# Kernel tuning notes

Measured on AMD Instinct MI355X. Metric: run time of the kernel, lower is better.

## Reference

```python
import jax, jax.numpy as jnp
import numpy as np

B, N, D, H = 128, 256, 256, 4  # batch, atoms, feature dim (= fingerprint = input = output), heads
NEG_BIG = -1e10


def setup_inputs() -> dict:
    key = jax.random.key(0)
    ks = jax.random.split(key, 8)
    atom_neighbor_SNN = jax.random.normal(ks[0], (B, N, D), dtype=jnp.float32)
    # 0/1 adjacency (float): mask trick exp(x*-1e10)*-1e10 expects binary entries
    x_full_atom_neighbors = jax.random.randint(ks[1], (B, N, N), 0, 2).astype(jnp.float32)
    # shared neighbor_fc: Linear(D, D)
    lim = 1.0 / np.sqrt(D)
    fc_w = jax.random.uniform(ks[2], (D, D), jnp.float32, -lim, lim)
    fc_b = jnp.zeros((D,), jnp.float32)
    # per-head kernels (xavier_uniform)
    xav = np.sqrt(6.0 / (D + D))
    kernels = jax.random.uniform(ks[3], (H, D, D), jnp.float32, -xav, xav)
    # attention kernels (2D, 1) split into self/neigh halves, xavier on (2D,1)
    xav_a = np.sqrt(6.0 / (2 * D + 1))
    att_self = jax.random.uniform(ks[4], (H, D), jnp.float32, -xav_a, xav_a)
    att_neigh = jax.random.uniform(ks[5], (H, D), jnp.float32, -xav_a, xav_a)
    epsilons = jnp.full((H,), 0.6, jnp.float32)
    biases = jnp.zeros((H, D), jnp.float32)
    att_biases = jnp.zeros((H,), jnp.float32)
    return {
        "atom_neighbor_SNN": atom_neighbor_SNN,
        "x_full_atom_neighbors": x_full_atom_neighbors,
        "fc_w": fc_w, "fc_b": fc_b,
        "kernels": kernels,
        "att_self": att_self, "att_neigh": att_neigh,
        "epsilons": epsilons, "biases": biases, "att_biases": att_biases,
    }


def reference(atom_neighbor_SNN, x_full_atom_neighbors, fc_w, fc_b, kernels,
              att_self, att_neigh, epsilons, biases, att_biases):
    x = x_full_atom_neighbors                      # [B,N,N]
    atom = atom_neighbor_SNN                       # [B,N,D]
    diag = jnp.diagonal(x, axis1=-2, axis2=-1)     # [B,N]
    # new_x[h] = x + eye*diag*(eps[h]-1); so new_x[h] @ atom = x@atom + (eps[h]-1)*diag[:,:,None]*atom
    base = jnp.einsum('bnm,bmd->bnd', x, atom)     # [B,N,D]
    diagterm = diag[..., None] * atom              # [B,N,D]
    nf = base[None] + (epsilons - 1.0)[:, None, None, None] * diagterm[None]  # [H,B,N,D]
    h = jax.nn.leaky_relu(jnp.einsum('hbnd,df->hbnf', nf, fc_w) + fc_b, 0.01)  # shared fc, leaky_relu
    feat = jnp.einsum('hbnf,hfo->hbno', h, kernels) + biases[:, None, None, :]  # [H,B,N,D]
    a_s = jnp.einsum('hbno,ho->hbn', feat, att_self) + att_biases[:, None, None]
    a_n = jnp.einsum('hbno,ho->hbn', feat, att_neigh)
    att = jax.nn.elu(a_s[..., :, None] + a_n[..., None, :])  # [H,B,N,N]
    mask = jnp.exp(x * NEG_BIG) * NEG_BIG                     # 0 on edges, -1e10 off edges
    att = jax.nn.softmax(att + mask[None], axis=-1)
    # dropout: identity (eval mode)
    node = jnp.einsum('hbij,hbjo->hbio', att, feat)           # [H,B,N,D]
    out = jnp.moveaxis(node, 0, 2).reshape(node.shape[1], node.shape[2], H * node.shape[3])  # concat heads -> [B,N,H*D]
    return out, att[-1]
```

## Files before the change

kernel.cpp:

```cpp
#include <hip/hip_runtime.h>

typedef __attribute__((ext_vector_type(8))) short bf16x8;
typedef __attribute__((ext_vector_type(4))) short short4v;
typedef __attribute__((ext_vector_type(4))) float f32x4;


__device__ __forceinline__ float b2f(short s){
  unsigned u = ((unsigned)(unsigned short)s) << 16;
  return __builtin_bit_cast(float, u);
}
__device__ __forceinline__ short f2b(float f){
  unsigned u = __builtin_bit_cast(unsigned, f);
  u = (u + 0x7FFFu + ((u >> 16) & 1u)) >> 16;
  return (short)(unsigned short)u;
}

#define SWZ(row, bytecol) ((((row) * 512) + (bytecol)) ^ (((row) & 7) << 4))

__global__ __launch_bounds__(256) void ktrans(const float* __restrict__ fcw, const float* __restrict__ kers,
                                              short* __restrict__ WT, short* __restrict__ KhT){
  __shared__ float tile[32][33];
  int z = blockIdx.z;
  const float* src = (z == 0) ? fcw : (kers + (z-1)*65536);
  short* dst = (z == 0) ? WT : (KhT + (z-1)*65536);
  int x0 = blockIdx.x*32, y0 = blockIdx.y*32;
  int tx = threadIdx.x & 31, ty = threadIdx.x >> 5;
  #pragma unroll
  for (int i = 0; i < 32; i += 8) tile[ty+i][tx] = src[(y0+ty+i)*256 + x0+tx];
  __syncthreads();
  #pragma unroll
  for (int i = 0; i < 32; i += 8) dst[(x0+ty+i)*256 + y0+tx] = f2b(tile[tx][ty+i]);
}

__global__ __launch_bounds__(512, 1) void kG12(const short* __restrict__ WT, const float* __restrict__ atom,
                                               const float* __restrict__ x,
                                               short* __restrict__ G2nf, short* __restrict__ G1,
                                               unsigned* __restrict__ xbits, float* __restrict__ diag){
  __shared__ __align__(16) char G2s[65536];
  int wg = blockIdx.x;
  int xcd = wg & 7, idx = wg >> 3;
  int b  = xcd + ((idx >> 1) << 3);
  int fh = idx & 1;
  int tid = threadIdx.x, lane = tid & 63, w = tid >> 6;
  int lr = lane & 15, lq = lane >> 4, koff = lq * 8;

  {
    int wm = (w >> 1) * 64, wf = (w & 1) * 64;
    const float* Ab = atom + b*65536;
    const short* Bw = WT + (fh*128 + wf)*256;
    f32x4 acc[4][4] = {};
    for (int k0 = 0; k0 < 256; k0 += 32){
      bf16x8 af[4], bfr[4];
      #pragma unroll
      for (int i = 0; i < 4; i++){
        const float* p = Ab + (wm + i*16 + lr)*256 + k0 + koff;
        f32x4 a0 = *(const f32x4*)p, a1 = *(const f32x4*)(p + 4);
        #pragma unroll
        for (int e = 0; e < 4; e++){ af[i][e] = f2b(a0[e]); af[i][4+e] = f2b(a1[e]); }
      }
      #pragma unroll
      for (int j = 0; j < 4; j++) bfr[j] = *(const bf16x8*)(Bw + (j*16 + lr)*256 + k0 + koff);
      #pragma unroll
      for (int i = 0; i < 4; i++)
        #pragma unroll
        for (int j = 0; j < 4; j++)
          acc[i][j] = __builtin_amdgcn_mfma_f32_16x16x32_bf16(af[i], bfr[j], acc[i][j], 0, 0, 0);
    }
    #pragma unroll
    for (int i = 0; i < 4; i++)
      #pragma unroll
      for (int j = 0; j < 4; j++){
        short4v v;
        #pragma unroll
        for (int r = 0; r < 4; r++) v[r] = f2b(acc[i][j][r]);
        int fl = wf + j*16 + lr;
        int m0 = wm + i*16 + lq*4;
        *(short4v*)(G2s + SWZ(fl, m0*2)) = v;
        #pragma unroll
        for (int r = 0; r < 4; r++)
          G2nf[b*65536 + (m0 + r)*256 + fh*128 + fl] = v[r];
      }
  }
  __syncthreads();

  {
    int wf2 = (w >> 2) * 64, wn2 = (w & 3) * 64;
    const float* Xb = x + b*65536;
    f32x4 acc[4][4] = {};
    for (int k0 = 0; k0 < 256; k0 += 32){
      bf16x8 af[4], bfr[4];
      #pragma unroll
      for (int i = 0; i < 4; i++) af[i]  = *(const bf16x8*)(G2s + SWZ(wf2 + i*16 + lr, (k0 + koff)*2));
      #pragma unroll
      for (int j = 0; j < 4; j++){
        int n = wn2 + j*16 + lr;
        const float* p = Xb + n*256 + k0 + koff;
        f32x4 x0 = *(const f32x4*)p, x1 = *(const f32x4*)(p + 4);
        unsigned b8 = 0u;
        #pragma unroll
        for (int e = 0; e < 4; e++){
          bfr[j][e] = f2b(x0[e]);     if (x0[e] > 0.5f) b8 |= (1u << e);
          bfr[j][4+e] = f2b(x1[e]);   if (x1[e] > 0.5f) b8 |= (1u << (4 + e));
        }
        if (w < 4){
          unsigned full = b8 << (lq * 8);
          full |= __shfl_xor(full, 16);
          full |= __shfl_xor(full, 32);
          if (lq == 0) xbits[(b*256 + n)*8 + (k0 >> 5)] = full;
          int nm = n & 31;
          if ((n & ~31) == k0 && (nm >> 3) == lq)
            diag[b*256 + n] = (nm & 4) ? x1[nm & 3] : x0[nm & 3];
        }
      }
      #pragma unroll
      for (int i = 0; i < 4; i++)
        #pragma unroll
        for (int j = 0; j < 4; j++)
          acc[i][j] = __builtin_amdgcn_mfma_f32_16x16x32_bf16(af[i], bfr[j], acc[i][j], 0, 0, 0);
    }
    #pragma unroll
    for (int i = 0; i < 4; i++)
      #pragma unroll
      for (int j = 0; j < 4; j++){
        short4v v;
        #pragma unroll
        for (int r = 0; r < 4; r++) v[r] = f2b(acc[i][j][r]);
        *(short4v*)(G1 + b*65536 + (wn2 + j*16 + lr)*256 + fh*128 + wf2 + i*16 + lq*4) = v;
      }
  }
}

__global__ __launch_bounds__(512, 1) void kHead(const short* __restrict__ KhT, const short* __restrict__ G1,
                                                const short* __restrict__ G2nf, const float* __restrict__ diag,
                                                const float* __restrict__ fcb, const float* __restrict__ epsv,
                                                const float* __restrict__ biases, const float* __restrict__ atts,
                                                const float* __restrict__ attn, const float* __restrict__ attbv,
                                                const unsigned* __restrict__ xbits,
                                                float* __restrict__ out, float* __restrict__ out2){
  __shared__ __align__(16) char featS[131072];
  __shared__ __align__(16) char scratch[24576];
  __shared__ float asvL[256], anvL[256], fcbL[256];

  short (*h1s)[40] = (short(*)[40])scratch;
  float (*red_s)[64] = (float(*)[64])(scratch);
  float (*red_n)[64] = (float(*)[64])(scratch + 2048);
  unsigned* xbitsL = (unsigned*)(scratch + 4096);

  int wg = blockIdx.x;
  int xcd = wg & 7, idx = wg >> 3;
  int b = xcd + ((idx >> 2) << 3);
  int h = idx & 3;
  int tid = threadIdx.x, lane = tid & 63, w = tid >> 6;
  float epsm1 = epsv[h] - 1.0f;
  const short* KA  = KhT + h*65536;
  const short* G1b = G1  + b*65536;
  const short* G2b = G2nf + b*65536;

  {
    int o = tid >> 1, half = (tid & 1) * 128;
    #pragma unroll
    for (int q = 0; q < 16; q++){
      int kk = half + q*8;
      bf16x8 v = *(const bf16x8*)(KA + o*256 + kk);
      *(bf16x8*)(featS + SWZ(o, kk*2)) = v;
    }
    if (tid < 256) fcbL[tid] = fcb[tid];
  }

  int nl = tid >> 1, rkk = (tid & 1) * 16;
  float cj = epsm1 * diag[b*256 + nl];

  int wro = (w >> 2) * 128;
  int wn  = (w & 3) * 64;
  int lr = lane & 15, lq = lane >> 4;
  int koff = lq * 8;

  bf16x8 p1a = *(const bf16x8*)(G1b + nl*256 + rkk);
  bf16x8 p1b = *(const bf16x8*)(G1b + nl*256 + rkk + 8);
  bf16x8 p2a = *(const bf16x8*)(G2b + nl*256 + rkk);
  bf16x8 p2b = *(const bf16x8*)(G2b + nl*256 + rkk + 8);

  __syncthreads();

  f32x4 acc[4][8] = {};
  for (int t = 0; t < 8; t++){
    int k0 = t*32;
    {
      bf16x8 o1, o2;
      #pragma unroll
      for (int e = 0; e < 8; e++){
        float v = b2f(p1a[e]) + cj*b2f(p2a[e]) + fcbL[k0 + rkk + e];
        v = v > 0.f ? v : 0.01f*v;
        o1[e] = f2b(v);
      }
      #pragma unroll
      for (int e = 0; e < 8; e++){
        float v = b2f(p1b[e]) + cj*b2f(p2b[e]) + fcbL[k0 + rkk + 8 + e];
        v = v > 0.f ? v : 0.01f*v;
        o2[e] = f2b(v);
      }
      *(bf16x8*)&h1s[nl][rkk] = o1;
      *(bf16x8*)&h1s[nl][rkk + 8] = o2;
    }
    __syncthreads();
    if (t < 7){
      int kn = k0 + 32;
      p1a = *(const bf16x8*)(G1b + nl*256 + kn + rkk);
      p1b = *(const bf16x8*)(G1b + nl*256 + kn + rkk + 8);
      p2a = *(const bf16x8*)(G2b + nl*256 + kn + rkk);
      p2b = *(const bf16x8*)(G2b + nl*256 + kn + rkk + 8);
    }
    bf16x8 af[4];
    #pragma unroll
    for (int j = 0; j < 4; j++) af[j] = *(const bf16x8*)&h1s[wn + j*16 + lr][koff];
    #pragma unroll
    for (int i = 0; i < 8; i++){
      bf16x8 bfv = *(const bf16x8*)(featS + SWZ(wro + i*16 + lr, (k0 + koff)*2));
      #pragma unroll
      for (int j = 0; j < 4; j++)
        acc[j][i] = __builtin_amdgcn_mfma_f32_16x16x32_bf16(af[j], bfv, acc[j][i], 0, 0, 0);
    }
    __syncthreads();
  }

  float ps[4][4] = {}, pn[4][4] = {};
  #pragma unroll
  for (int i = 0; i < 8; i++){
    int od = wro + i*16 + lr;
    float bi  = biases[h*256 + od];
    float wsv = atts[h*256 + od];
    float wnv = attn[h*256 + od];
    #pragma unroll
    for (int j = 0; j < 4; j++){
      short4v sv;
      #pragma unroll
      for (int r = 0; r < 4; r++){
        float fv = acc[j][i][r] + bi;
        sv[r] = f2b(fv);
        ps[j][r] += fv * wsv;
        pn[j][r] += fv * wnv;
      }
      *(short4v*)(featS + SWZ(od, (wn + j*16 + lq*4)*2) ) = sv;
    }
  }
  #pragma unroll
  for (int j = 0; j < 4; j++)
    #pragma unroll
    for (int r = 0; r < 4; r++){
      float s = ps[j][r], nv = pn[j][r];
      s += __shfl_xor(s, 1); s += __shfl_xor(s, 2); s += __shfl_xor(s, 4); s += __shfl_xor(s, 8);
      nv += __shfl_xor(nv, 1); nv += __shfl_xor(nv, 2); nv += __shfl_xor(nv, 4); nv += __shfl_xor(nv, 8);
      ps[j][r] = s; pn[j][r] = nv;
    }
  if (lr == 0){
    #pragma unroll
    for (int j = 0; j < 4; j++)
      #pragma unroll
      for (int r = 0; r < 4; r++){
        red_s[w][j*16 + lq*4 + r] = ps[j][r];
        red_n[w][j*16 + lq*4 + r] = pn[j][r];
      }
  }
  {
    const unsigned* xb = xbits + b*2048;
    #pragma unroll
    for (int q = 0; q < 4; q++) xbitsL[tid*4 + q] = xb[tid*4 + q];
  }
  __syncthreads();
  if (tid < 256){
    int q = tid >> 6, nn = tid & 63;
    asvL[tid] = red_s[q][nn] + red_s[q+4][nn] + attbv[h];
    anvL[tid] = red_n[q][nn] + red_n[q+4][nn];
  }
  __syncthreads();

  int wi = w * 32;
  bf16x8 bfp[2][8];
  #pragma unroll
  for (int sub = 0; sub < 2; sub++){
    int i = wi + sub*16 + lr;
    float as_i = asvL[i];
    float Lv[8][8];
    float mx = -3.0e38f;
    #pragma unroll
    for (int t = 0; t < 8; t++){
      unsigned bits = xbitsL[i*8 + t] >> (lq*8);
      #pragma unroll
      for (int e = 0; e < 8; e++){
        float s = as_i + anvL[t*32 + lq*8 + e];
        float el = s > 0.f ? s : (__expf(s) - 1.0f);
        float L = el + (((bits >> e) & 1u) ? 0.f : -1.0e10f);
        Lv[t][e] = L; mx = fmaxf(mx, L);
      }
    }
    mx = fmaxf(mx, __shfl_xor(mx, 16));
    mx = fmaxf(mx, __shfl_xor(mx, 32));
    float sum = 0.f;
    #pragma unroll
    for (int t = 0; t < 8; t++)
      #pragma unroll
      for (int e = 0; e < 8; e++){ float p = __expf(Lv[t][e] - mx); Lv[t][e] = p; sum += p; }
    sum += __shfl_xor(sum, 16);
    sum += __shfl_xor(sum, 32);
    float inv = 1.0f / sum;
    #pragma unroll
    for (int t = 0; t < 8; t++){
      bf16x8 pv;
      #pragma unroll
      for (int e = 0; e < 8; e++) pv[e] = f2b(Lv[t][e] * inv);
      bfp[sub][t] = pv;
    }
    if (h == 3){
      float* o2 = out2 + b*65536 + i*256 + lq*8;
      #pragma unroll
      for (int t = 0; t < 8; t++){
        f32x4 v0, v1;
        #pragma unroll
        for (int e = 0; e < 4; e++){ v0[e] = Lv[t][e]*inv; v1[e] = Lv[t][4+e]*inv; }
        *(f32x4*)(o2 + t*32) = v0;
        *(f32x4*)(o2 + t*32 + 4) = v1;
      }
    }
  }

  float* outb = out + (size_t)(b*256 + wi)*1024 + h*256;
  #pragma unroll 1
  for (int ot = 0; ot < 16; ot++){
    f32x4 a2[2] = {};
    #pragma unroll
    for (int t = 0; t < 8; t++){
      bf16x8 afv = *(const bf16x8*)(featS + SWZ(ot*16 + lr, (t*32 + lq*8)*2));
      a2[0] = __builtin_amdgcn_mfma_f32_16x16x32_bf16(afv, bfp[0][t], a2[0], 0, 0, 0);
      a2[1] = __builtin_amdgcn_mfma_f32_16x16x32_bf16(afv, bfp[1][t], a2[1], 0, 0, 0);
    }
    *(f32x4*)(outb + (size_t)(lr)*1024 + ot*16 + lq*4) = a2[0];
    *(f32x4*)(outb + (size_t)(16 + lr)*1024 + ot*16 + lq*4) = a2[1];
  }
}

extern "C" void kernel_launch(void* const* d_in, const int* in_sizes, int n_in,
                              void* d_out, int out_size, void* d_ws, size_t ws_size,
                              hipStream_t stream) {
  const float* atom   = (const float*)d_in[0];
  const float* x      = (const float*)d_in[1];
  const float* fc_w   = (const float*)d_in[2];
  const float* fc_b   = (const float*)d_in[3];
  const float* kers   = (const float*)d_in[4];
  const float* att_s  = (const float*)d_in[5];
  const float* att_n  = (const float*)d_in[6];
  const float* eps    = (const float*)d_in[7];
  const float* biases = (const float*)d_in[8];
  const float* att_b  = (const float*)d_in[9];

  char* w = (char*)d_ws;
  short* WT      = (short*)(w);
  short* KhT     = (short*)(w + 131072);
  float* diag    = (float*)(w + 655360);
  unsigned* xbits= (unsigned*)(w + 786432);
  short* G2nf    = (short*)(w + 1835008);
  short* G1      = (short*)(w + 18612224);

  float* out  = (float*)d_out;
  float* out2 = out + 33554432;

  ktrans<<<dim3(8, 8, 5), 256, 0, stream>>>(fc_w, kers, WT, KhT);
  kG12<<<dim3(256), 512, 0, stream>>>(WT, atom, x, G2nf, G1, xbits, diag);
  kHead<<<dim3(512), 512, 0, stream>>>(KhT, G1, G2nf, diag, fc_b, eps,
                                       biases, att_s, att_n, att_b, xbits, out, out2);
}
```

Baseline: 145.2 us.

## Split G12 over feature quarters and stage full activation tile in LDS for head GEMM

kG12 now splits the feature dimension into quarters instead of halves. That doubles the grid to 512 workgroups, halves the LDS staging buffer, and declares higher occupancy through launch bounds. kHead now computes the full leaky-relu activation tile (all 256 k) into LDS once up front and reads the per-head kernel weights straight from global memory. Previously the weights were staged in LDS and the activations were produced 32 columns at a time with two barriers per k-step. This removes the per-iteration synchronisation, at the cost of uncached global weight loads inside the MFMA loop and redundant recomputation of the atom-by-weight GEMM across the quarter splits.

```diff
diff --git a/kernel.cpp b/kernel.cpp
--- a/kernel.cpp
+++ b/kernel.cpp
@@ -32,25 +32,25 @@
   for (int i = 0; i < 32; i += 8) dst[(x0+ty+i)*256 + y0+tx] = f2b(tile[tx][ty+i]);
 }
 
-__global__ __launch_bounds__(512, 1) void kG12(const short* __restrict__ WT, const float* __restrict__ atom,
+__global__ __launch_bounds__(512, 4) void kG12(const short* __restrict__ WT, const float* __restrict__ atom,
                                                const float* __restrict__ x,
                                                short* __restrict__ G2nf, short* __restrict__ G1,
                                                unsigned* __restrict__ xbits, float* __restrict__ diag){
-  __shared__ __align__(16) char G2s[65536];
+  __shared__ __align__(16) char G2s[32768];
   int wg = blockIdx.x;
   int xcd = wg & 7, idx = wg >> 3;
-  int b  = xcd + ((idx >> 1) << 3);
-  int fh = idx & 1;
+  int b  = xcd + ((idx >> 2) << 3);
+  int fq = idx & 3;
   int tid = threadIdx.x, lane = tid & 63, w = tid >> 6;
   int lr = lane & 15, lq = lane >> 4, koff = lq * 8;
 
   {
-    int wm = (w >> 1) * 64, wf = (w & 1) * 64;
+    int wm = (w >> 1) * 64, wf = (w & 1) * 32;
     const float* Ab = atom + b*65536;
-    const short* Bw = WT + (fh*128 + wf)*256;
-    f32x4 acc[4][4] = {};
+    const short* Bw = WT + (fq*64 + wf)*256;
+    f32x4 acc[4][2] = {};
     for (int k0 = 0; k0 < 256; k0 += 32){
-      bf16x8 af[4], bfr[4];
+      bf16x8 af[4], bfr[2];
       #pragma unroll
       for (int i = 0; i < 4; i++){
         const float* p = Ab + (wm + i*16 + lr)*256 + k0 + koff;
@@ -59,17 +59,17 @@
         for (int e = 0; e < 4; e++){ af[i][e] = f2b(a0[e]); af[i][4+e] = f2b(a1[e]); }
       }
       #pragma unroll
-      for (int j = 0; j < 4; j++) bfr[j] = *(const bf16x8*)(Bw + (j*16 + lr)*256 + k0 + koff);
+      for (int j = 0; j < 2; j++) bfr[j] = *(const bf16x8*)(Bw + (j*16 + lr)*256 + k0 + koff);
       #pragma unroll
       for (int i = 0; i < 4; i++)
         #pragma unroll
-        for (int j = 0; j < 4; j++)
+        for (int j = 0; j < 2; j++)
           acc[i][j] = __builtin_amdgcn_mfma_f32_16x16x32_bf16(af[i], bfr[j], acc[i][j], 0, 0, 0);
     }
     #pragma unroll
     for (int i = 0; i < 4; i++)
       #pragma unroll
-      for (int j = 0; j < 4; j++){
+      for (int j = 0; j < 2; j++){
         short4v v;
         #pragma unroll
         for (int r = 0; r < 4; r++) v[r] = f2b(acc[i][j][r]);
@@ -78,19 +78,19 @@
         *(short4v*)(G2s + SWZ(fl, m0*2)) = v;
         #pragma unroll
         for (int r = 0; r < 4; r++)
-          G2nf[b*65536 + (m0 + r)*256 + fh*128 + fl] = v[r];
+          G2nf[b*65536 + (m0 + r)*256 + fq*64 + fl] = v[r];
       }
   }
   __syncthreads();
 
   {
-    int wf2 = (w >> 2) * 64, wn2 = (w & 3) * 64;
+    int wf2 = (w >> 2) * 32, wn2 = (w & 3) * 64;
     const float* Xb = x + b*65536;
-    f32x4 acc[4][4] = {};
+    f32x4 acc[2][4] = {};
     for (int k0 = 0; k0 < 256; k0 += 32){
-      bf16x8 af[4], bfr[4];
-      #pragma unroll
-      for (int i = 0; i < 4; i++) af[i]  = *(const bf16x8*)(G2s + SWZ(wf2 + i*16 + lr, (k0 + koff)*2));
+      bf16x8 af[2], bfr[4];
+      #pragma unroll
+      for (int i = 0; i < 2; i++) af[i] = *(const bf16x8*)(G2s + SWZ(wf2 + i*16 + lr, (k0 + koff)*2));
       #pragma unroll
       for (int j = 0; j < 4; j++){
         int n = wn2 + j*16 + lr;
@@ -113,19 +113,19 @@
         }
       }
       #pragma unroll
-      for (int i = 0; i < 4; i++)
+      for (int i = 0; i < 2; i++)
         #pragma unroll
         for (int j = 0; j < 4; j++)
           acc[i][j] = __builtin_amdgcn_mfma_f32_16x16x32_bf16(af[i], bfr[j], acc[i][j], 0, 0, 0);
     }
     #pragma unroll
-    for (int i = 0; i < 4; i++)
+    for (int i = 0; i < 2; i++)
       #pragma unroll
       for (int j = 0; j < 4; j++){
         short4v v;
         #pragma unroll
         for (int r = 0; r < 4; r++) v[r] = f2b(acc[i][j][r]);
-        *(short4v*)(G1 + b*65536 + (wn2 + j*16 + lr)*256 + fh*128 + wf2 + i*16 + lq*4) = v;
+        *(short4v*)(G1 + b*65536 + (wn2 + j*16 + lr)*256 + fq*64 + wf2 + i*16 + lq*4) = v;
       }
   }
 }
@@ -138,10 +138,9 @@
                                                 const unsigned* __restrict__ xbits,
                                                 float* __restrict__ out, float* __restrict__ out2){
   __shared__ __align__(16) char featS[131072];
-  __shared__ __align__(16) char scratch[24576];
-  __shared__ float asvL[256], anvL[256], fcbL[256];
-
-  short (*h1s)[40] = (short(*)[40])scratch;
+  __shared__ __align__(16) char scratch[12288];
+  __shared__ float asvL[256], anvL[256];
+
   float (*red_s)[64] = (float(*)[64])(scratch);
   float (*red_n)[64] = (float(*)[64])(scratch + 2048);
   unsigned* xbitsL = (unsigned*)(scratch + 4096);
@@ -157,71 +156,61 @@
   const short* G2b = G2nf + b*65536;
 
   {
-    int o = tid >> 1, half = (tid & 1) * 128;
-    #pragma unroll
-    for (int q = 0; q < 16; q++){
-      int kk = half + q*8;
-      bf16x8 v = *(const bf16x8*)(KA + o*256 + kk);
-      *(bf16x8*)(featS + SWZ(o, kk*2)) = v;
-    }
-    if (tid < 256) fcbL[tid] = fcb[tid];
-  }
-
-  int nl = tid >> 1, rkk = (tid & 1) * 16;
-  float cj = epsm1 * diag[b*256 + nl];
+    int nl = tid >> 1, rkk = (tid & 1) * 16;
+    float cj = epsm1 * diag[b*256 + nl];
+    #pragma unroll
+    for (int kb = 0; kb < 8; kb++){
+      int k0 = kb*32 + rkk;
+      bf16x8 g1a = *(const bf16x8*)(G1b + nl*256 + k0);
+      bf16x8 g1c = *(const bf16x8*)(G1b + nl*256 + k0 + 8);
+      bf16x8 g2a = *(const bf16x8*)(G2b + nl*256 + k0);
+      bf16x8 g2c = *(const bf16x8*)(G2b + nl*256 + k0 + 8);
+      f32x4 f0 = *(const f32x4*)(fcb + k0);
+      f32x4 f1 = *(const f32x4*)(fcb + k0 + 4);
+      f32x4 f2 = *(const f32x4*)(fcb + k0 + 8);
+      f32x4 f3 = *(const f32x4*)(fcb + k0 + 12);
+      bf16x8 o1, o2;
+      #pragma unroll
+      for (int e = 0; e < 8; e++){
+        float v = b2f(g1a[e]) + cj*b2f(g2a[e]) + ((e < 4) ? f0[e] : f1[e-4]);
+        v = v > 0.f ? v : 0.01f*v;
+        o1[e] = f2b(v);
+      }
+      #pragma unroll
+      for (int e = 0; e < 8; e++){
+        float v = b2f(g1c[e]) + cj*b2f(g2c[e]) + ((e < 4) ? f2[e] : f3[e-4]);
+        v = v > 0.f ? v : 0.01f*v;
+        o2[e] = f2b(v);
+      }
+      *(bf16x8*)(featS + SWZ(nl, k0*2)) = o1;
+      *(bf16x8*)(featS + SWZ(nl, k0*2 + 16)) = o2;
+    }
+    const unsigned* xb = xbits + b*2048;
+    #pragma unroll
+    for (int q = 0; q < 4; q++) xbitsL[tid*4 + q] = xb[tid*4 + q];
+  }
+  __syncthreads();
 
   int wro = (w >> 2) * 128;
   int wn  = (w & 3) * 64;
   int lr = lane & 15, lq = lane >> 4;
   int koff = lq * 8;
 
-  bf16x8 p1a = *(const bf16x8*)(G1b + nl*256 + rkk);
-  bf16x8 p1b = *(const bf16x8*)(G1b + nl*256 + rkk + 8);
-  bf16x8 p2a = *(const bf16x8*)(G2b + nl*256 + rkk);
-  bf16x8 p2b = *(const bf16x8*)(G2b + nl*256 + rkk + 8);
-
-  __syncthreads();
-
   f32x4 acc[4][8] = {};
   for (int t = 0; t < 8; t++){
     int k0 = t*32;
-    {
-      bf16x8 o1, o2;
-      #pragma unroll
-      for (int e = 0; e < 8; e++){
-        float v = b2f(p1a[e]) + cj*b2f(p2a[e]) + fcbL[k0 + rkk + e];
-        v = v > 0.f ? v : 0.01f*v;
-        o1[e] = f2b(v);
-      }
-      #pragma unroll
-      for (int e = 0; e < 8; e++){
-        float v = b2f(p1b[e]) + cj*b2f(p2b[e]) + fcbL[k0 + rkk + 8 + e];
-        v = v > 0.f ? v : 0.01f*v;
-        o2[e] = f2b(v);
-      }
-      *(bf16x8*)&h1s[nl][rkk] = o1;
-      *(bf16x8*)&h1s[nl][rkk + 8] = o2;
-    }
-    __syncthreads();
-    if (t < 7){
-      int kn = k0 + 32;
-      p1a = *(const bf16x8*)(G1b + nl*256 + kn + rkk);
-      p1b = *(const bf16x8*)(G1b + nl*256 + kn + rkk + 8);
-      p2a = *(const bf16x8*)(G2b + nl*256 + kn + rkk);
-      p2b = *(const bf16x8*)(G2b + nl*256 + kn + rkk + 8);
-    }
     bf16x8 af[4];
     #pragma unroll
-    for (int j = 0; j < 4; j++) af[j] = *(const bf16x8*)&h1s[wn + j*16 + lr][koff];
+    for (int j = 0; j < 4; j++) af[j] = *(const bf16x8*)(featS + SWZ(wn + j*16 + lr, (k0 + koff)*2));
     #pragma unroll
     for (int i = 0; i < 8; i++){
-      bf16x8 bfv = *(const bf16x8*)(featS + SWZ(wro + i*16 + lr, (k0 + koff)*2));
+      bf16x8 bfv = *(const bf16x8*)(KA + (wro + i*16 + lr)*256 + k0 + koff);
       #pragma unroll
       for (int j = 0; j < 4; j++)
         acc[j][i] = __builtin_amdgcn_mfma_f32_16x16x32_bf16(af[j], bfv, acc[j][i], 0, 0, 0);
     }
-    __syncthreads();
-  }
+  }
+  __syncthreads();
 
   float ps[4][4] = {}, pn[4][4] = {};
   #pragma unroll
@@ -260,11 +249,6 @@
         red_s[w][j*16 + lq*4 + r] = ps[j][r];
         red_n[w][j*16 + lq*4 + r] = pn[j][r];
       }
-  }
-  {
-    const unsigned* xb = xbits + b*2048;
-    #pragma unroll
-    for (int q = 0; q < 4; q++) xbitsL[tid*4 + q] = xb[tid*4 + q];
   }
   __syncthreads();
   if (tid < 256){
@@ -364,7 +348,7 @@
   float* out2 = out + 33554432;
 
   ktrans<<<dim3(8, 8, 5), 256, 0, stream>>>(fc_w, kers, WT, KhT);
-  kG12<<<dim3(256), 512, 0, stream>>>(WT, atom, x, G2nf, G1, xbits, diag);
+  kG12<<<dim3(512), 512, 0, stream>>>(WT, atom, x, G2nf, G1, xbits, diag);
   kHead<<<dim3(512), 512, 0, stream>>>(KhT, G1, G2nf, diag, fc_b, eps,
                                        biases, att_s, att_n, att_b, xbits, out, out2);
 }
```

Measured after the change: 179.4 us. +23.5%, slower.
